# Kernel optimization log

Measured on AMD Instinct MI355X. Metric: run time of the kernel, lower is better.

The kernel has to match this reference:

```python
import jax, jax.numpy as jnp
import numpy as np

N = 8192        # num nodes
E = 262144      # num edges (avg degree 32)
IN_DIM = 256
OUT_DIM = 256
NEG_SLOPE = 0.2


def setup_inputs() -> dict:
    key = jax.random.key(0)
    k1, k2, k3, k4 = jax.random.split(key, 4)
    x = jax.random.normal(k1, (N, IN_DIM), dtype=jnp.float32)
    edge_index = jax.random.randint(k2, (2, E), 0, N, dtype=jnp.int64)
    # learned params: W of Linear(in_dim,out_dim,bias=False) stored as (in_dim,out_dim),
    # attn Linear(2*out_dim,1,bias=False) stored as flat vector a of shape (2*out_dim,)
    W = jax.random.normal(k3, (IN_DIM, OUT_DIM), dtype=jnp.float32) * (1.0 / np.sqrt(IN_DIM))
    a = jax.random.normal(k4, (2 * OUT_DIM,), dtype=jnp.float32) * (1.0 / np.sqrt(2 * OUT_DIM))
    return {"x": x, "edge_index": edge_index, "W": W, "a": a}


def reference(x, edge_index, W, a):
    # h = W(x): (N, out_dim)
    h = x @ W
    src, tgt = edge_index[0], edge_index[1]
    # attn(cat(h[src], h[tgt])) == h[src] @ a_src + h[tgt] @ a_tgt
    a_src, a_tgt = a[:OUT_DIM], a[OUT_DIM:]
    e = jax.nn.leaky_relu(h[src] @ a_src + h[tgt] @ a_tgt, negative_slope=NEG_SLOPE)  # (E,)
    # faithful to original: scatter scores into dense (N,N) zeros, dense softmax over rows
    alpha = jnp.zeros((N, N), dtype=x.dtype).at[src, tgt].set(e)
    alpha = jax.nn.softmax(alpha, axis=-1)
    # dropout is identity in eval / p=0
    out = alpha @ h  # (N, out_dim)
    return out
```

## Files before the change

### kernel.cpp

```cpp
#include <hip/hip_runtime.h>
#include <math.h>

#define N_NODES 8192
#define E_EDGES 262144
#define DIM 256
#define NEG_SLOPE 0.2f
#define ROW_CAP 128

typedef __attribute__((ext_vector_type(8))) short short8;
typedef __attribute__((ext_vector_type(4))) float f32x4;

#define OFF_HB       0u
#define OFF_XB       4194304u
#define OFF_WT       8388608u
#define OFF_CURSOR   8519680u
#define OFF_SV       8552448u
#define OFF_TV       8585216u
#define OFF_SALL     8617984u
#define ZERO_BASE    OFF_CURSOR
#define ZERO_BYTES   99328u
#define ZERO_VEC4    6208u
#define OFF_CSR      8620032u

__device__ __forceinline__ unsigned f2bf(float f) {
  unsigned u = __float_as_uint(f);
  u += 0x7fffu + ((u >> 16) & 1u);
  return u >> 16;
}

__global__ __launch_bounds__(256) void setup_kernel(const float* __restrict__ x,
                                                    const float* __restrict__ W,
                                                    unsigned short* __restrict__ xb,
                                                    unsigned short* __restrict__ wt,
                                                    float4* __restrict__ zero_p) {
  const int b = blockIdx.x;
  const int t = threadIdx.x;
  if (b < 1024) {
    const int i = b * 2048 + t * 8;
    const float4 v0 = *(const float4*)(x + i);
    const float4 v1 = *(const float4*)(x + i + 4);
    uint4 o;
    o.x = f2bf(v0.x) | (f2bf(v0.y) << 16);
    o.y = f2bf(v0.z) | (f2bf(v0.w) << 16);
    o.z = f2bf(v1.x) | (f2bf(v1.y) << 16);
    o.w = f2bf(v1.z) | (f2bf(v1.w) << 16);
    *(uint4*)(xb + i) = o;
  } else if (b < 1088) {
    const int idx = (b - 1024) * 1024 + t * 4;
    const int n = idx >> 8;
    const int k = idx & 255;
    uint2 o;
    o.x = f2bf(W[(size_t)k * DIM + n]) | (f2bf(W[(size_t)(k + 1) * DIM + n]) << 16);
    o.y = f2bf(W[(size_t)(k + 2) * DIM + n]) | (f2bf(W[(size_t)(k + 3) * DIM + n]) << 16);
    *(uint2*)(wt + idx) = o;
  } else {
    const unsigned i = (b - 1088) * 256 + t;
    if (i < ZERO_VEC4) zero_p[i] = float4{0.f, 0.f, 0.f, 0.f};
  }
}

__global__ __launch_bounds__(256) void gemm_scatter_kernel(const unsigned short* __restrict__ xb,
                                                           const unsigned short* __restrict__ wt,
                                                           const float* __restrict__ a,
                                                           unsigned short* __restrict__ hb,
                                                           float* __restrict__ sv,
                                                           float* __restrict__ tv,
                                                           float* __restrict__ S_all,
                                                           const int* __restrict__ ei,
                                                           int* __restrict__ cursor,
                                                           int* __restrict__ csr) {
  const int bid = blockIdx.x;
  if (bid >= 256) {
    const int k = (bid - 256) * 256 + threadIdx.x;
    const int src = ei[k];
    const int tgt = ei[E_EDGES + k];
    const int pos = atomicAdd(&cursor[src], 1);
    if (pos < ROW_CAP) csr[src * ROW_CAP + pos] = tgt;
    return;
  }
  __shared__ unsigned short Al[128 * 64];
  __shared__ unsigned short Bl[64 * 64];
  const int bx = bid >> 2, by = bid & 3;
  const int m0 = bx * 128, n0 = by * 64;
  const int t = threadIdx.x;
  const int w = t >> 6, l = t & 63;
  const int q = l >> 4, l15 = l & 15;

  f32x4 acc[2][4] = {{{0.f,0.f,0.f,0.f},{0.f,0.f,0.f,0.f},{0.f,0.f,0.f,0.f},{0.f,0.f,0.f,0.f}},
                     {{0.f,0.f,0.f,0.f},{0.f,0.f,0.f,0.f},{0.f,0.f,0.f,0.f},{0.f,0.f,0.f,0.f}}};

  const int lrow = l >> 3;
  const int kvs = (l & 7) ^ lrow;

  for (int ki = 0; ki < 4; ++ki) {
    const int k0 = ki * 64;
#pragma unroll
    for (int o = 0; o < 4; ++o) {
      const int op = w * 4 + o;
      const unsigned short* gp = xb + (size_t)(m0 + op * 8 + lrow) * DIM + k0 + kvs * 8;
      __builtin_amdgcn_global_load_lds((const __attribute__((address_space(1))) unsigned*)gp,
                                       (__attribute__((address_space(3))) unsigned*)(Al + op * 512),
                                       16, 0, 0);
    }
#pragma unroll
    for (int o = 0; o < 2; ++o) {
      const int op = w * 2 + o;
      const unsigned short* gp = wt + (size_t)(n0 + op * 8 + lrow) * DIM + k0 + kvs * 8;
      __builtin_amdgcn_global_load_lds((const __attribute__((address_space(1))) unsigned*)gp,
                                       (__attribute__((address_space(3))) unsigned*)(Bl + op * 512),
                                       16, 0, 0);
    }
    __syncthreads();
#pragma unroll
    for (int s = 0; s < 2; ++s) {
      const int kv = s * 4 + q;
      short8 af[2], bf[4];
#pragma unroll
      for (int mi = 0; mi < 2; ++mi) {
        const int m = w * 32 + mi * 16 + l15;
        af[mi] = *(const short8*)(Al + m * 64 + ((kv ^ (m & 7)) * 8));
      }
#pragma unroll
      for (int nt = 0; nt < 4; ++nt) {
        const int n = nt * 16 + l15;
        bf[nt] = *(const short8*)(Bl + n * 64 + ((kv ^ (n & 7)) * 8));
      }
#pragma unroll
      for (int mi = 0; mi < 2; ++mi)
#pragma unroll
        for (int nt = 0; nt < 4; ++nt)
          acc[mi][nt] = __builtin_amdgcn_mfma_f32_16x16x32_bf16(af[mi], bf[nt], acc[mi][nt], 0, 0, 0);
    }
    __syncthreads();
  }

  float asv[4], atv[4];
#pragma unroll
  for (int nt = 0; nt < 4; ++nt) {
    const int n = n0 + nt * 16 + l15;
    asv[nt] = a[n];
    atv[nt] = a[DIM + n];
  }
#pragma unroll
  for (int mi = 0; mi < 2; ++mi)
#pragma unroll
    for (int r = 0; r < 4; ++r) {
      float sp = 0.f, tp = 0.f;
#pragma unroll
      for (int nt = 0; nt < 4; ++nt) {
        const float v = acc[mi][nt][r];
        sp += v * asv[nt];
        tp += v * atv[nt];
      }
#pragma unroll
      for (int off = 1; off < 16; off <<= 1) {
        sp += __shfl_xor(sp, off);
        tp += __shfl_xor(tp, off);
      }
      if (l15 == 0) {
        const int m = m0 + w * 32 + mi * 16 + q * 4 + r;
        atomicAdd(&sv[m], sp);
        atomicAdd(&tv[m], tp);
      }
    }
#pragma unroll
  for (int nt = 0; nt < 4; ++nt) {
    float cs = 0.f;
#pragma unroll
    for (int mi = 0; mi < 2; ++mi)
#pragma unroll
      for (int r = 0; r < 4; ++r) cs += acc[mi][nt][r];
    cs += __shfl_xor(cs, 16);
    cs += __shfl_xor(cs, 32);
    if (q == 0) atomicAdd(&S_all[n0 + nt * 16 + l15], cs);
  }
#pragma unroll
  for (int mi = 0; mi < 2; ++mi)
#pragma unroll
    for (int r = 0; r < 4; ++r) {
      const int m = m0 + w * 32 + mi * 16 + q * 4 + r;
#pragma unroll
      for (int nt = 0; nt < 4; ++nt)
        hb[(size_t)m * DIM + n0 + nt * 16 + l15] = (unsigned short)f2bf(acc[mi][nt][r]);
    }
}

__global__ __launch_bounds__(256) void row_kernel(const unsigned short* __restrict__ hb,
                                                  const float* __restrict__ sv,
                                                  const float* __restrict__ tv,
                                                  const float* __restrict__ S_all,
                                                  const int* __restrict__ cursor,
                                                  const int* __restrict__ csr,
                                                  float* __restrict__ out) {
  __shared__ unsigned bm[4][256];
  const int w = threadIdx.x >> 6;
  const int lane = threadIdx.x & 63;
  const int row = blockIdx.x * 4 + w;
#pragma unroll
  for (int i = lane; i < 256; i += 64) bm[w][i] = 0u;
  __syncthreads();

  const int n_total = min(cursor[row], ROW_CAP);
  const float srow = sv[row];

  float4 acc = {0.f, 0.f, 0.f, 0.f};
  float Z = 0.f;

  for (int e0 = 0; e0 < n_total; e0 += 64) {
    const int cn = min(64, n_total - e0);
    float wgt = 0.f;
    int tg = 0;
    if (lane < cn) {
      tg = csr[row * ROW_CAP + e0 + lane];
      const unsigned msk = 1u << (tg & 31);
      const unsigned old = atomicOr(&bm[w][tg >> 5], msk);
      if (!(old & msk)) {
        float ev = srow + tv[tg];
        ev = (ev > 0.f) ? ev : NEG_SLOPE * ev;
        wgt = expm1f(ev);
      }
    }
    for (int j = 0; j < cn; j += 8) {
#pragma unroll
      for (int u = 0; u < 8; ++u) {
        const float wj = __shfl(wgt, j + u);
        const int tj = __shfl(tg, j + u);
        const uint2 p = *(const uint2*)(hb + (size_t)tj * DIM + (lane << 2));
        acc.x += wj * __uint_as_float(p.x << 16);
        acc.y += wj * __uint_as_float(p.x & 0xffff0000u);
        acc.z += wj * __uint_as_float(p.y << 16);
        acc.w += wj * __uint_as_float(p.y & 0xffff0000u);
        Z += wj;
      }
    }
  }

  const float4 sa = *(const float4*)(S_all + (lane << 2));
  const float inv = 1.0f / ((float)N_NODES + Z);
  float4 o;
  o.x = (sa.x + acc.x) * inv;
  o.y = (sa.y + acc.y) * inv;
  o.z = (sa.z + acc.z) * inv;
  o.w = (sa.w + acc.w) * inv;
  *(float4*)(out + (size_t)row * DIM + (lane << 2)) = o;
}

extern "C" void kernel_launch(void* const* d_in, const int* in_sizes, int n_in,
                              void* d_out, int out_size, void* d_ws, size_t ws_size,
                              hipStream_t stream) {
  const float* x = (const float*)d_in[0];
  const int* ei = (const int*)d_in[1];
  const float* W = (const float*)d_in[2];
  const float* a = (const float*)d_in[3];
  float* out = (float*)d_out;

  unsigned char* ws = (unsigned char*)d_ws;
  unsigned short* hb = (unsigned short*)(ws + OFF_HB);
  unsigned short* xb = (unsigned short*)(ws + OFF_XB);
  unsigned short* wt = (unsigned short*)(ws + OFF_WT);
  int* cursor = (int*)(ws + OFF_CURSOR);
  float* sv = (float*)(ws + OFF_SV);
  float* tv = (float*)(ws + OFF_TV);
  float* S_all = (float*)(ws + OFF_SALL);
  int* csr = (int*)(ws + OFF_CSR);

  setup_kernel<<<1113, 256, 0, stream>>>(x, W, xb, wt, (float4*)(ws + ZERO_BASE));
  gemm_scatter_kernel<<<1280, 256, 0, stream>>>(xb, wt, a, hb, sv, tv, S_all, ei, cursor, csr);
  row_kernel<<<N_NODES / 4, 256, 0, stream>>>(hb, sv, tv, S_all, cursor, csr, out);
}
```

Before: 104.7 us.

## Double-buffer GEMM LDS tiles, halve scatter blocks, use readlane in row aggregation

The GEMM main loop now double-buffers its A/B LDS tiles, issuing the next k-slice load before computing on the current one, with a single waitcnt+barrier per iteration instead of two syncthreads. The edge-scatter blocks each handle two edges per thread, so the grid shrinks from 1280 to 768 blocks. In row_kernel the broadcasts use readlane instead of shfl, the per-edge Z sum becomes one per-lane sum plus a final butterfly reduction, and a syncthreads after the bitmap clear is removed. That removal is safe only because each wave clears and uses its own bitmap row. The double buffer doubles LDS use per block, which may lower occupancy.

```diff
diff --git a/kernel.cpp b/kernel.cpp
--- a/kernel.cpp
+++ b/kernel.cpp
@@ -71,15 +71,19 @@
                                                            int* __restrict__ csr) {
   const int bid = blockIdx.x;
   if (bid >= 256) {
-    const int k = (bid - 256) * 256 + threadIdx.x;
-    const int src = ei[k];
-    const int tgt = ei[E_EDGES + k];
-    const int pos = atomicAdd(&cursor[src], 1);
-    if (pos < ROW_CAP) csr[src * ROW_CAP + pos] = tgt;
+    const int k0e = (bid - 256) * 256 + threadIdx.x;
+#pragma unroll
+    for (int h = 0; h < 2; ++h) {
+      const int k = k0e + h * 131072;
+      const int src = ei[k];
+      const int tgt = ei[E_EDGES + k];
+      const int pos = atomicAdd(&cursor[src], 1);
+      if (pos < ROW_CAP) csr[src * ROW_CAP + pos] = tgt;
+    }
     return;
   }
-  __shared__ unsigned short Al[128 * 64];
-  __shared__ unsigned short Bl[64 * 64];
+  __shared__ unsigned short Al[2][128 * 64];
+  __shared__ unsigned short Bl[2][64 * 64];
   const int bx = bid >> 2, by = bid & 3;
   const int m0 = bx * 128, n0 = by * 64;
   const int t = threadIdx.x;
@@ -92,14 +96,14 @@
   const int lrow = l >> 3;
   const int kvs = (l & 7) ^ lrow;
 
-  for (int ki = 0; ki < 4; ++ki) {
+  auto stage = [&](int ki, int buf) {
     const int k0 = ki * 64;
 #pragma unroll
     for (int o = 0; o < 4; ++o) {
       const int op = w * 4 + o;
       const unsigned short* gp = xb + (size_t)(m0 + op * 8 + lrow) * DIM + k0 + kvs * 8;
       __builtin_amdgcn_global_load_lds((const __attribute__((address_space(1))) unsigned*)gp,
-                                       (__attribute__((address_space(3))) unsigned*)(Al + op * 512),
+                                       (__attribute__((address_space(3))) unsigned*)(&Al[buf][op * 512]),
                                        16, 0, 0);
     }
 #pragma unroll
@@ -107,10 +111,17 @@
       const int op = w * 2 + o;
       const unsigned short* gp = wt + (size_t)(n0 + op * 8 + lrow) * DIM + k0 + kvs * 8;
       __builtin_amdgcn_global_load_lds((const __attribute__((address_space(1))) unsigned*)gp,
-                                       (__attribute__((address_space(3))) unsigned*)(Bl + op * 512),
+                                       (__attribute__((address_space(3))) unsigned*)(&Bl[buf][op * 512]),
                                        16, 0, 0);
     }
-    __syncthreads();
+  };
+
+  stage(0, 0);
+  int buf = 0;
+  for (int ki = 0; ki < 4; ++ki) {
+    asm volatile("s_waitcnt vmcnt(0)" ::: "memory");
+    __builtin_amdgcn_s_barrier();
+    if (ki < 3) stage(ki + 1, buf ^ 1);
 #pragma unroll
     for (int s = 0; s < 2; ++s) {
       const int kv = s * 4 + q;
@@ -118,12 +129,12 @@
 #pragma unroll
       for (int mi = 0; mi < 2; ++mi) {
         const int m = w * 32 + mi * 16 + l15;
-        af[mi] = *(const short8*)(Al + m * 64 + ((kv ^ (m & 7)) * 8));
+        af[mi] = *(const short8*)(&Al[buf][m * 64 + ((kv ^ (m & 7)) * 8)]);
       }
 #pragma unroll
       for (int nt = 0; nt < 4; ++nt) {
         const int n = nt * 16 + l15;
-        bf[nt] = *(const short8*)(Bl + n * 64 + ((kv ^ (n & 7)) * 8));
+        bf[nt] = *(const short8*)(&Bl[buf][n * 64 + ((kv ^ (n & 7)) * 8)]);
       }
 #pragma unroll
       for (int mi = 0; mi < 2; ++mi)
@@ -131,7 +142,7 @@
         for (int nt = 0; nt < 4; ++nt)
           acc[mi][nt] = __builtin_amdgcn_mfma_f32_16x16x32_bf16(af[mi], bf[nt], acc[mi][nt], 0, 0, 0);
     }
-    __syncthreads();
+    buf ^= 1;
   }
 
   float asv[4], atv[4];
@@ -198,13 +209,12 @@
   const int row = blockIdx.x * 4 + w;
 #pragma unroll
   for (int i = lane; i < 256; i += 64) bm[w][i] = 0u;
-  __syncthreads();
 
   const int n_total = min(cursor[row], ROW_CAP);
   const float srow = sv[row];
 
   float4 acc = {0.f, 0.f, 0.f, 0.f};
-  float Z = 0.f;
+  float zacc = 0.f;
 
   for (int e0 = 0; e0 < n_total; e0 += 64) {
     const int cn = min(64, n_total - e0);
@@ -220,23 +230,27 @@
         wgt = expm1f(ev);
       }
     }
+    zacc += wgt;
     for (int j = 0; j < cn; j += 8) {
 #pragma unroll
       for (int u = 0; u < 8; ++u) {
-        const float wj = __shfl(wgt, j + u);
-        const int tj = __shfl(tg, j + u);
+        const int tj = __builtin_amdgcn_readlane(tg, j + u);
+        const float wj = __uint_as_float(
+            (unsigned)__builtin_amdgcn_readlane((int)__float_as_uint(wgt), j + u));
         const uint2 p = *(const uint2*)(hb + (size_t)tj * DIM + (lane << 2));
         acc.x += wj * __uint_as_float(p.x << 16);
         acc.y += wj * __uint_as_float(p.x & 0xffff0000u);
         acc.z += wj * __uint_as_float(p.y << 16);
         acc.w += wj * __uint_as_float(p.y & 0xffff0000u);
-        Z += wj;
-      }
-    }
-  }
+      }
+    }
+  }
+
+#pragma unroll
+  for (int off = 1; off < 64; off <<= 1) zacc += __shfl_xor(zacc, off);
 
   const float4 sa = *(const float4*)(S_all + (lane << 2));
-  const float inv = 1.0f / ((float)N_NODES + Z);
+  const float inv = 1.0f / ((float)N_NODES + zacc);
   float4 o;
   o.x = (sa.x + acc.x) * inv;
   o.y = (sa.y + acc.y) * inv;
@@ -265,6 +279,6 @@
   int* csr = (int*)(ws + OFF_CSR);
 
   setup_kernel<<<1113, 256, 0, stream>>>(x, W, xb, wt, (float4*)(ws + ZERO_BASE));
-  gemm_scatter_kernel<<<1280, 256, 0, stream>>>(xb, wt, a, hb, sv, tv, S_all, ei, cursor, csr);
+  gemm_scatter_kernel<<<768, 256, 0, stream>>>(xb, wt, a, hb, sv, tv, S_all, ei, cursor, csr);
   row_kernel<<<N_NODES / 4, 256, 0, stream>>>(hb, sv, tv, S_all, cursor, csr, out);
 }
```

After: 104.8 us. Within noise of the previous version (+0.1%).
